# Optimization experiments

Measured on AMD Instinct MI355X. Metric: run time of the kernel, lower is better.

The kernel has to match this reference:

```python
import jax, jax.numpy as jnp
import numpy as np

B, S, H = 32, 2048, 1024


def setup_inputs() -> dict:
    key = jax.random.key(0)
    ks = jax.random.split(key, 8)
    scale = 1.0 / np.sqrt(H)
    return {
        "query": jax.random.normal(ks[0], (B, 1, H), dtype=jnp.float32),
        "keys": jax.random.normal(ks[1], (B, S, H), dtype=jnp.float32),
        "Wa_w": jax.random.uniform(ks[2], (H, H), jnp.float32, -scale, scale),
        "Wa_b": jax.random.uniform(ks[3], (H,), jnp.float32, -scale, scale),
        "Ua_w": jax.random.uniform(ks[4], (H, H), jnp.float32, -scale, scale),
        "Ua_b": jax.random.uniform(ks[5], (H,), jnp.float32, -scale, scale),
        "Va_w": jax.random.uniform(ks[6], (1, H), jnp.float32, -scale, scale),
        "Va_b": jax.random.uniform(ks[7], (1,), jnp.float32, -scale, scale),
        "idx": 0,
    }


def reference(query, keys, Wa_w, Wa_b, Ua_w, Ua_b, Va_w, Va_b, idx):
    # torch Linear: y = x @ W.T + b
    q_proj = jnp.einsum("bqh,oh->bqo", query, Wa_w) + Wa_b   # (B,1,H)
    k_proj = jnp.einsum("bsh,oh->bso", keys, Ua_w) + Ua_b    # (B,S,H)
    energy = jnp.tanh(q_proj + k_proj)                        # (B,S,H) broadcast over S
    scores = jnp.einsum("bsh,h->bs", energy, Va_w[0]) + Va_b[0]  # (B,S)
    weights = jax.nn.softmax(scores, axis=-1)[:, None, :]     # (B,1,S)
    context = jnp.einsum("bqs,bsh->bqh", weights, keys)       # (B,1,H)
    return (context, weights)
```

## Files before the change

kernel.cpp:

```cpp
#include <hip/hip_runtime.h>
#include <hip/hip_bf16.h>
#include <math.h>


#define B_ 32
#define S_ 2048
#define H_ 1024
#define M_ (B_ * S_)

#define QP_BLOCKS 512
#define UA_BLOCKS 32

typedef __bf16 bf16x8 __attribute__((ext_vector_type(8)));
typedef float floatx4 __attribute__((ext_vector_type(4)));

__device__ inline unsigned bf16_rne(float f) {
  unsigned u = __builtin_bit_cast(unsigned, f);
  return (u + 0x7fffu + ((u >> 16) & 1u)) >> 16;
}
__device__ inline unsigned pk2(float x, float y) {
  return bf16_rne(x) | (bf16_rne(y) << 16);
}
__device__ inline unsigned cvtpk(float x, float y) {
  unsigned r;
  asm("v_cvt_pk_bf16_f32 %0, %1, %2" : "=v"(r) : "v"(x), "v"(y));
  return r;
}

__device__ inline float fast_tanh(float x) {
  const float xc = fminf(fmaxf(x, -8.f), 8.f);
  const float e = __expf(2.f * xc);
  return (e - 1.f) * __builtin_amdgcn_rcpf(e + 1.f);
}

#define GLDS(g, l)                                                    \
  __builtin_amdgcn_global_load_lds(                                   \
      (const __attribute__((address_space(1))) void*)(g),             \
      (__attribute__((address_space(3))) void*)(l), 16, 0, 0)

__device__ inline uint4 conv8(const float4* s2) {
  const float4 a = s2[0], b = s2[1];
  uint4 o;
  o.x = pk2(a.x, a.y); o.y = pk2(a.z, a.w);
  o.z = pk2(b.x, b.y); o.w = pk2(b.z, b.w);
  return o;
}

__global__ __launch_bounds__(256) void prep_kernel(
    const float* __restrict__ Ua_w, const float* __restrict__ query,
    const float* __restrict__ Wa_w, const float* __restrict__ Wa_b,
    const float* __restrict__ Ua_b, unsigned short* __restrict__ ubf,
    float* __restrict__ qp, int do_ua) {
  const int blk = blockIdx.x;
  const int tid = threadIdx.x;
  if (blk < QP_BLOCKS) {
    const int b = blk >> 4;
    const int os = (blk & 15) * 64;
    const int lane = tid & 63;
    const int w = tid >> 6;
    __shared__ float qsh[H_];
    *(float4*)&qsh[tid * 4] = *(const float4*)(query + (size_t)b * H_ + tid * 4);
    __syncthreads();
    for (int t = 0; t < 16; ++t) {
      const int o = os + w * 16 + t;
      const float* wr = Wa_w + (size_t)o * H_;
      float p = 0.f;
#pragma unroll
      for (int j = 0; j < 16; ++j) p += wr[lane + 64 * j] * qsh[lane + 64 * j];
#pragma unroll
      for (int m = 32; m; m >>= 1) p += __shfl_xor(p, m);
      if (lane == 0) qp[b * H_ + o] = p + Wa_b[o] + Ua_b[o];
    }
  } else {
    if (!do_ua) return;
    const int tg = (blk - QP_BLOCKS) * 256 + tid;
#pragma unroll
    for (int c = 0; c < 16; ++c) {
      const size_t idx = (size_t)c * 8192 + tg;
      ((uint4*)ubf)[idx] = conv8((const float4*)Ua_w + idx * 2);
    }
  }
}

__device__ inline void swizzle_rc(int idx, int& rb, int& cb) {
  cb = (idx >> 3) & 7;
  rb = (idx & 7) | ((idx >> 6) << 3);
}
__device__ inline int chunk_f(int r) { return (r & 3) ^ ((r >> 2) & 3); }

__global__ __launch_bounds__(256) void scores_af32_kernel(
    const float* __restrict__ keys, const unsigned short* __restrict__ ubf,
    const float* __restrict__ qp, const float* __restrict__ Va_w,
    float* __restrict__ sp) {
  const int tid = threadIdx.x;
  int rb, cb;
  swizzle_rc(blockIdx.x, rb, cb);
  const int row0 = rb * 128, c0 = cb * 128;
  const int bq = row0 >> 11;
  const int lane = tid & 63;
  const int w = tid >> 6;
  const int wm = w >> 1, wn = w & 1;
  const int q4 = lane >> 4, n16 = lane & 15;

  __shared__ __align__(16) unsigned short Asm[128][32];
  __shared__ __align__(16) unsigned short Bsm[128][32];
  __shared__ float red[2][128];

  floatx4 acc[4][4];
#pragma unroll
  for (int i = 0; i < 4; ++i)
#pragma unroll
    for (int j = 0; j < 4; ++j) acc[i][j] = {0.f, 0.f, 0.f, 0.f};

  const int r0a = w * 32;
  const int lr = lane >> 2;
  const int lc = ((lane & 3) ^ chunk_f(lr)) * 8;
  const unsigned short* gB0 = ubf + (size_t)(c0 + r0a + lr) * H_ + lc;
  const unsigned short* gB1 = ubf + (size_t)(c0 + r0a + 16 + lr) * H_ + lc;
  unsigned short* lB0 = &Bsm[r0a][0];
  unsigned short* lB1 = &Bsm[r0a + 16][0];

  const int ar = tid >> 1;
  const int ac0 = (tid & 1) * 2;
  const float* gA = keys + (size_t)(row0 + ar) * H_ + ac0 * 8;
  unsigned short* lA0 = &Asm[ar][((ac0 ^ chunk_f(ar)) & 3) * 8];
  unsigned short* lA1 = &Asm[ar][(((ac0 + 1) ^ chunk_f(ar)) & 3) * 8];

  const int fn = chunk_f(n16);

  float4 a0 = *(const float4*)(gA + 0);
  float4 a1 = *(const float4*)(gA + 4);
  float4 a2 = *(const float4*)(gA + 8);
  float4 a3 = *(const float4*)(gA + 12);

  for (int kt = 0; kt < 32; ++kt) {
    const int k0 = kt * 32;
    __syncthreads();
    GLDS(gB0 + k0, lB0);
    GLDS(gB1 + k0, lB1);
    uint4 u0, u1;
    u0.x = cvtpk(a0.x, a0.y); u0.y = cvtpk(a0.z, a0.w);
    u0.z = cvtpk(a1.x, a1.y); u0.w = cvtpk(a1.z, a1.w);
    u1.x = cvtpk(a2.x, a2.y); u1.y = cvtpk(a2.z, a2.w);
    u1.z = cvtpk(a3.x, a3.y); u1.w = cvtpk(a3.z, a3.w);
    *(uint4*)lA0 = u0;
    *(uint4*)lA1 = u1;
    const int kn = ((kt + 1) & 31) * 32;
    a0 = *(const float4*)(gA + kn + 0);
    a1 = *(const float4*)(gA + kn + 4);
    a2 = *(const float4*)(gA + kn + 8);
    a3 = *(const float4*)(gA + kn + 12);
    __syncthreads();
    bf16x8 af[4], bfr[4];
#pragma unroll
    for (int i = 0; i < 4; ++i)
      af[i] = *(const bf16x8*)&Asm[wm * 64 + i * 16 + n16][(q4 ^ fn) * 8];
#pragma unroll
    for (int j = 0; j < 4; ++j)
      bfr[j] = *(const bf16x8*)&Bsm[wn * 64 + j * 16 + n16][(q4 ^ fn) * 8];
#pragma unroll
    for (int i = 0; i < 4; ++i)
#pragma unroll
      for (int j = 0; j < 4; ++j)
        acc[i][j] = __builtin_amdgcn_mfma_f32_16x16x32_bf16(af[i], bfr[j], acc[i][j], 0, 0, 0);
  }

  float rsum[4][4];
#pragma unroll
  for (int i = 0; i < 4; ++i)
#pragma unroll
    for (int r = 0; r < 4; ++r) rsum[i][r] = 0.f;
#pragma unroll
  for (int j = 0; j < 4; ++j) {
    const int col = c0 + wn * 64 + j * 16 + n16;
    const float qv = qp[bq * H_ + col];
    const float vv = Va_w[col];
#pragma unroll
    for (int i = 0; i < 4; ++i)
#pragma unroll
      for (int r = 0; r < 4; ++r)
        rsum[i][r] += fast_tanh(acc[i][j][r] + qv) * vv;
  }
#pragma unroll
  for (int i = 0; i < 4; ++i)
#pragma unroll
    for (int r = 0; r < 4; ++r) {
      float v = rsum[i][r];
      v += __shfl_xor(v, 1);
      v += __shfl_xor(v, 2);
      v += __shfl_xor(v, 4);
      v += __shfl_xor(v, 8);
      rsum[i][r] = v;
    }
  if (n16 == 0) {
#pragma unroll
    for (int i = 0; i < 4; ++i)
#pragma unroll
      for (int r = 0; r < 4; ++r)
        red[wn][wm * 64 + i * 16 + q4 * 4 + r] = rsum[i][r];
  }
  __syncthreads();
  if (tid < 128) sp[(size_t)cb * M_ + row0 + tid] = red[0][tid] + red[1][tid];
}

__global__ __launch_bounds__(256) void scores_f32_kernel(
    const float* __restrict__ keys, const float* __restrict__ Ua_w,
    const float* __restrict__ qp, const float* __restrict__ Va_w,
    float* __restrict__ sp) {
  const int tid = threadIdx.x;
  int rb, cb;
  swizzle_rc(blockIdx.x, rb, cb);
  const int row0 = rb * 128, c0 = cb * 128;
  const int bq = row0 >> 11;
  const int lane = tid & 63;
  const int w = tid >> 6;
  const int wm = w >> 1, wn = w & 1;
  const int q4 = lane >> 4, n16 = lane & 15;

  __shared__ __align__(16) unsigned short Asm[128][40];
  __shared__ __align__(16) unsigned short Bsm[128][40];
  __shared__ float red[2][128];

  floatx4 acc[4][4];
#pragma unroll
  for (int i = 0; i < 4; ++i)
#pragma unroll
    for (int j = 0; j < 4; ++j) acc[i][j] = {0.f, 0.f, 0.f, 0.f};

  for (int kt = 0; kt < 32; ++kt) {
    const int k0 = kt * 32;
    __syncthreads();
#pragma unroll
    for (int rep = 0; rep < 4; ++rep) {
      const int idx4 = rep * 256 + tid;
      const int r = idx4 >> 3;
      const int c4 = (idx4 & 7) << 2;
      const float4 va = *(const float4*)(keys + (size_t)(row0 + r) * H_ + k0 + c4);
      *(uint2*)&Asm[r][c4] = make_uint2(pk2(va.x, va.y), pk2(va.z, va.w));
      const float4 vb = *(const float4*)(Ua_w + (size_t)(c0 + r) * H_ + k0 + c4);
      *(uint2*)&Bsm[r][c4] = make_uint2(pk2(vb.x, vb.y), pk2(vb.z, vb.w));
    }
    __syncthreads();
    bf16x8 af[4], bfr[4];
#pragma unroll
    for (int i = 0; i < 4; ++i)
      af[i] = *(const bf16x8*)&Asm[wm * 64 + i * 16 + n16][q4 * 8];
#pragma unroll
    for (int j = 0; j < 4; ++j)
      bfr[j] = *(const bf16x8*)&Bsm[wn * 64 + j * 16 + n16][q4 * 8];
#pragma unroll
    for (int i = 0; i < 4; ++i)
#pragma unroll
      for (int j = 0; j < 4; ++j)
        acc[i][j] = __builtin_amdgcn_mfma_f32_16x16x32_bf16(af[i], bfr[j], acc[i][j], 0, 0, 0);
  }

  float rsum[4][4];
#pragma unroll
  for (int i = 0; i < 4; ++i)
#pragma unroll
    for (int r = 0; r < 4; ++r) rsum[i][r] = 0.f;
#pragma unroll
  for (int j = 0; j < 4; ++j) {
    const int col = c0 + wn * 64 + j * 16 + n16;
    const float qv = qp[bq * H_ + col];
    const float vv = Va_w[col];
#pragma unroll
    for (int i = 0; i < 4; ++i)
#pragma unroll
      for (int r = 0; r < 4; ++r)
        rsum[i][r] += fast_tanh(acc[i][j][r] + qv) * vv;
  }
#pragma unroll
  for (int i = 0; i < 4; ++i)
#pragma unroll
    for (int r = 0; r < 4; ++r) {
      float v = rsum[i][r];
      v += __shfl_xor(v, 1);
      v += __shfl_xor(v, 2);
      v += __shfl_xor(v, 4);
      v += __shfl_xor(v, 8);
      rsum[i][r] = v;
    }
  if (n16 == 0) {
#pragma unroll
    for (int i = 0; i < 4; ++i)
#pragma unroll
      for (int r = 0; r < 4; ++r)
        red[wn][wm * 64 + i * 16 + q4 * 4 + r] = rsum[i][r];
  }
  __syncthreads();
  if (tid < 128) sp[(size_t)cb * M_ + row0 + tid] = red[0][tid] + red[1][tid];
}

__global__ __launch_bounds__(256) void softmax_kernel(
    const float* __restrict__ sp, float* __restrict__ sw) {
  const int b = blockIdx.x, tid = threadIdx.x;
  float v[8];
#pragma unroll
  for (int k = 0; k < 8; ++k) {
    const size_t base = (size_t)b * S_ + tid + 256 * k;
    float s = 0.f;
#pragma unroll
    for (int j = 0; j < 8; ++j) s += sp[(size_t)j * M_ + base];
    v[k] = s;
  }
  float mx = v[0];
#pragma unroll
  for (int k = 1; k < 8; ++k) mx = fmaxf(mx, v[k]);
#pragma unroll
  for (int m = 32; m; m >>= 1) mx = fmaxf(mx, __shfl_xor(mx, m));
  __shared__ float sred[4], ssum[4];
  if ((tid & 63) == 0) sred[tid >> 6] = mx;
  __syncthreads();
  mx = fmaxf(fmaxf(sred[0], sred[1]), fmaxf(sred[2], sred[3]));
  float e[8], s = 0.f;
#pragma unroll
  for (int k = 0; k < 8; ++k) { e[k] = __expf(v[k] - mx); s += e[k]; }
#pragma unroll
  for (int m = 32; m; m >>= 1) s += __shfl_xor(s, m);
  if ((tid & 63) == 0) ssum[tid >> 6] = s;
  __syncthreads();
  s = ssum[0] + ssum[1] + ssum[2] + ssum[3];
  const float inv = 1.0f / s;
#pragma unroll
  for (int k = 0; k < 8; ++k) sw[b * S_ + tid + 256 * k] = e[k] * inv;
}

__global__ __launch_bounds__(256) void context1_kernel(
    const float* __restrict__ keys, const float* __restrict__ weights,
    float* __restrict__ pctx) {
  const int b = blockIdx.x >> 6;
  const int ch = blockIdx.x & 63;
  const int s0 = ch * 32;
  const int h4 = threadIdx.x;
  const float4* kp4 = (const float4*)(keys + (size_t)(b * S_ + s0) * H_) + h4;
  const float4* wp4 = (const float4*)(weights + b * S_ + s0);
  float4 acc = {0.f, 0.f, 0.f, 0.f};
#pragma unroll
  for (int sq = 0; sq < 8; ++sq) {
    const float4 wv = wp4[sq];
    const float4 k0 = kp4[(sq * 4 + 0) * 256];
    const float4 k1 = kp4[(sq * 4 + 1) * 256];
    const float4 k2 = kp4[(sq * 4 + 2) * 256];
    const float4 k3 = kp4[(sq * 4 + 3) * 256];
    acc.x += wv.x * k0.x + wv.y * k1.x + wv.z * k2.x + wv.w * k3.x;
    acc.y += wv.x * k0.y + wv.y * k1.y + wv.z * k2.y + wv.w * k3.y;
    acc.z += wv.x * k0.z + wv.y * k1.z + wv.z * k2.z + wv.w * k3.z;
    acc.w += wv.x * k0.w + wv.y * k1.w + wv.z * k2.w + wv.w * k3.w;
  }
  *(float4*)(pctx + ((size_t)(b * 64 + ch)) * H_ + h4 * 4) = acc;
}

__global__ __launch_bounds__(256) void context2_kernel(
    const float* __restrict__ pctx, float* __restrict__ ctx) {
  const int b = blockIdx.x;
  const int h4 = threadIdx.x * 4;
  float4 acc = {0.f, 0.f, 0.f, 0.f};
#pragma unroll 8
  for (int c = 0; c < 64; ++c) {
    const float4 v = *(const float4*)(pctx + ((size_t)(b * 64 + c)) * H_ + h4);
    acc.x += v.x; acc.y += v.y; acc.z += v.z; acc.w += v.w;
  }
  *(float4*)(ctx + b * H_ + h4) = acc;
}

extern "C" void kernel_launch(void* const* d_in, const int* in_sizes, int n_in,
                              void* d_out, int out_size, void* d_ws, size_t ws_size,
                              hipStream_t stream) {
  const float* query = (const float*)d_in[0];
  const float* keys  = (const float*)d_in[1];
  const float* Wa_w  = (const float*)d_in[2];
  const float* Wa_b  = (const float*)d_in[3];
  const float* Ua_w  = (const float*)d_in[4];
  const float* Ua_b  = (const float*)d_in[5];
  const float* Va_w  = (const float*)d_in[6];

  float* out = (float*)d_out;
  float* ctx = out;
  float* sw  = out + B_ * H_;

  const size_t qpb = (size_t)B_ * H_ * 4;
  const size_t spb = (size_t)8 * M_ * 4;
  const size_t pcb = (size_t)B_ * 64 * H_ * 4;
  const size_t ub  = (size_t)H_ * H_ * 2;
  float* qp = (float*)d_ws;
  float* sp = (float*)((char*)d_ws + qpb);
  float* pctx = (float*)((char*)d_ws + qpb + spb);
  unsigned short* ubf = (unsigned short*)((char*)d_ws + qpb + spb + pcb);
  const bool fast = ws_size >= qpb + spb + pcb + ub;

  prep_kernel<<<QP_BLOCKS + UA_BLOCKS, 256, 0, stream>>>(
      Ua_w, query, Wa_w, Wa_b, Ua_b, ubf, qp, fast ? 1 : 0);
  if (fast) {
    scores_af32_kernel<<<4096, 256, 0, stream>>>(keys, ubf, qp, Va_w, sp);
  } else {
    scores_f32_kernel<<<4096, 256, 0, stream>>>(keys, Ua_w, qp, Va_w, sp);
  }
  softmax_kernel<<<B_, 256, 0, stream>>>(sp, sw);
  context1_kernel<<<2048, 256, 0, stream>>>(keys, sw, pctx);
  context2_kernel<<<B_, 256, 0, stream>>>(pctx, ctx);
}
```

Baseline: 726.9 us.

## Double-buffer LDS tiles in scores GEMM to overlap loads with MFMA

Converts the A/B shared-memory tiles of the scores kernel into ping-pong buffers. The next K-tile's global loads (keys as fp32, Ua as bf16 via direct-to-LDS) are issued before the current tile's MFMAs, and the converted A tile is written into the other buffer afterwards. This cuts the loop to one barrier per iteration and is meant to hide global-load latency behind compute. In exchange it doubles LDS use, which may reduce occupancy, and adds a sched_barrier that constrains instruction scheduling.

```diff
diff --git a/kernel.cpp b/kernel.cpp
--- a/kernel.cpp
+++ b/kernel.cpp
@@ -102,9 +102,10 @@
   const int wm = w >> 1, wn = w & 1;
   const int q4 = lane >> 4, n16 = lane & 15;
 
-  __shared__ __align__(16) unsigned short Asm[128][32];
-  __shared__ __align__(16) unsigned short Bsm[128][32];
+  __shared__ __align__(16) unsigned short Asm[2][128][32];
+  __shared__ __align__(16) unsigned short Bsm[2][128][32];
   __shared__ float red[2][128];
+  const int BUFO = 128 * 32;
 
   floatx4 acc[4][4];
 #pragma unroll
@@ -117,14 +118,14 @@
   const int lc = ((lane & 3) ^ chunk_f(lr)) * 8;
   const unsigned short* gB0 = ubf + (size_t)(c0 + r0a + lr) * H_ + lc;
   const unsigned short* gB1 = ubf + (size_t)(c0 + r0a + 16 + lr) * H_ + lc;
-  unsigned short* lB0 = &Bsm[r0a][0];
-  unsigned short* lB1 = &Bsm[r0a + 16][0];
+  unsigned short* lB0 = &Bsm[0][r0a][0];
+  unsigned short* lB1 = &Bsm[0][r0a + 16][0];
 
   const int ar = tid >> 1;
   const int ac0 = (tid & 1) * 2;
   const float* gA = keys + (size_t)(row0 + ar) * H_ + ac0 * 8;
-  unsigned short* lA0 = &Asm[ar][((ac0 ^ chunk_f(ar)) & 3) * 8];
-  unsigned short* lA1 = &Asm[ar][(((ac0 + 1) ^ chunk_f(ar)) & 3) * 8];
+  unsigned short* lA0 = &Asm[0][ar][((ac0 ^ chunk_f(ar)) & 3) * 8];
+  unsigned short* lA1 = &Asm[0][ar][(((ac0 + 1) ^ chunk_f(ar)) & 3) * 8];
 
   const int fn = chunk_f(n16);
 
@@ -132,12 +133,9 @@
   float4 a1 = *(const float4*)(gA + 4);
   float4 a2 = *(const float4*)(gA + 8);
   float4 a3 = *(const float4*)(gA + 12);
-
-  for (int kt = 0; kt < 32; ++kt) {
-    const int k0 = kt * 32;
-    __syncthreads();
-    GLDS(gB0 + k0, lB0);
-    GLDS(gB1 + k0, lB1);
+  GLDS(gB0, lB0);
+  GLDS(gB1, lB1);
+  {
     uint4 u0, u1;
     u0.x = cvtpk(a0.x, a0.y); u0.y = cvtpk(a0.z, a0.w);
     u0.z = cvtpk(a1.x, a1.y); u0.w = cvtpk(a1.z, a1.w);
@@ -145,24 +143,44 @@
     u1.z = cvtpk(a3.x, a3.y); u1.w = cvtpk(a3.z, a3.w);
     *(uint4*)lA0 = u0;
     *(uint4*)lA1 = u1;
-    const int kn = ((kt + 1) & 31) * 32;
-    a0 = *(const float4*)(gA + kn + 0);
-    a1 = *(const float4*)(gA + kn + 4);
-    a2 = *(const float4*)(gA + kn + 8);
-    a3 = *(const float4*)(gA + kn + 12);
-    __syncthreads();
+  }
+  __syncthreads();
+
+  for (int kt = 0; kt < 32; ++kt) {
+    const int cur = kt & 1;
+    const int nxt = cur ^ 1;
+    if (kt < 31) {
+      const int kn = (kt + 1) * 32;
+      a0 = *(const float4*)(gA + kn + 0);
+      a1 = *(const float4*)(gA + kn + 4);
+      a2 = *(const float4*)(gA + kn + 8);
+      a3 = *(const float4*)(gA + kn + 12);
+      GLDS(gB0 + kn, lB0 + nxt * BUFO);
+      GLDS(gB1 + kn, lB1 + nxt * BUFO);
+    }
+    __builtin_amdgcn_sched_barrier(0);
     bf16x8 af[4], bfr[4];
 #pragma unroll
     for (int i = 0; i < 4; ++i)
-      af[i] = *(const bf16x8*)&Asm[wm * 64 + i * 16 + n16][(q4 ^ fn) * 8];
+      af[i] = *(const bf16x8*)(&Asm[0][wm * 64 + i * 16 + n16][(q4 ^ fn) * 8] + cur * BUFO);
 #pragma unroll
     for (int j = 0; j < 4; ++j)
-      bfr[j] = *(const bf16x8*)&Bsm[wn * 64 + j * 16 + n16][(q4 ^ fn) * 8];
+      bfr[j] = *(const bf16x8*)(&Bsm[0][wn * 64 + j * 16 + n16][(q4 ^ fn) * 8] + cur * BUFO);
 #pragma unroll
     for (int i = 0; i < 4; ++i)
 #pragma unroll
       for (int j = 0; j < 4; ++j)
         acc[i][j] = __builtin_amdgcn_mfma_f32_16x16x32_bf16(af[i], bfr[j], acc[i][j], 0, 0, 0);
+    if (kt < 31) {
+      uint4 u0, u1;
+      u0.x = cvtpk(a0.x, a0.y); u0.y = cvtpk(a0.z, a0.w);
+      u0.z = cvtpk(a1.x, a1.y); u0.w = cvtpk(a1.z, a1.w);
+      u1.x = cvtpk(a2.x, a2.y); u1.y = cvtpk(a2.z, a2.w);
+      u1.z = cvtpk(a3.x, a3.y); u1.w = cvtpk(a3.z, a3.w);
+      *(uint4*)(lA0 + nxt * BUFO) = u0;
+      *(uint4*)(lA1 + nxt * BUFO) = u1;
+    }
+    __syncthreads();
   }
 
   float rsum[4][4];
```

After: 693.2 us. 4.6% less time.
